# Kernel tuning notes

Measured on AMD Instinct MI355X. Metric: run time of the kernel, lower is better.

Reference implementation:

```python
import jax, jax.numpy as jnp
import numpy as np

TEMPERATURE = 0.07
EPS = 1e-12  # F.normalize eps


def setup_inputs() -> dict:
    key = jax.random.key(0)
    k1, k2 = jax.random.split(key)
    B, D = 4096, 1024
    return {
        "features_1": jax.random.normal(k1, (B, D), dtype=jnp.float32),
        "features_2": jax.random.normal(k2, (B, D), dtype=jnp.float32),
    }


def _l2_normalize(x):
    n = jnp.sqrt(jnp.sum(x * x, axis=1, keepdims=True))
    return x / jnp.maximum(n, EPS)


def reference(features_1, features_2):
    B = features_1.shape[0]
    f1 = _l2_normalize(features_1)
    f2 = _l2_normalize(features_2)
    f = jnp.concatenate([f1, f2], axis=0)  # [2B, D]
    # cosine sim of already-normalized vectors == plain matmul
    sim = (f @ f.T) / TEMPERATURE  # [2B, 2B]
    # denominator: logsumexp over each row excluding the diagonal (self-sim)
    eye = jnp.eye(2 * B, dtype=bool)
    lse = jax.nn.logsumexp(jnp.where(eye, -jnp.inf, sim), axis=1)  # [2B]
    # positives: cross-view pairs (i+B, i) then (i, i+B)
    idx = jnp.arange(B)
    pos = jnp.concatenate([sim[idx + B, idx], sim[idx, idx + B]], axis=0)  # [2B]
    loss = -jnp.mean(pos - lse)
    return loss
```

## Files before the change

kernel.cpp:

```cpp
#include <hip/hip_runtime.h>
#include <hip/hip_bf16.h>
#include <math.h>

#define INV_T (1.0f / 0.07f)

typedef __bf16 bf16x8 __attribute__((ext_vector_type(8)));
typedef float f32x4 __attribute__((ext_vector_type(4)));

__device__ __forceinline__ void gld16(const void* g, void* l) {
    __builtin_amdgcn_global_load_lds(
        (const __attribute__((address_space(1))) unsigned int*)g,
        (__attribute__((address_space(3))) unsigned int*)l,
        16, 0, 0);
}

__global__ __launch_bounds__(256) void norm_kernel(
    const float4* __restrict__ f1, const float4* __restrict__ f2,
    ushort4* __restrict__ F, float* __restrict__ S, float* __restrict__ P,
    int B) {
    const int i = blockIdx.x;
    const int t = threadIdx.x;

    float4 x = f1[i * 256 + t];
    float4 y = f2[i * 256 + t];

    float s1 = x.x * x.x + x.y * x.y + x.z * x.z + x.w * x.w;
    float s2 = y.x * y.x + y.y * y.y + y.z * y.z + y.w * y.w;
    float dd = x.x * y.x + x.y * y.y + x.z * y.z + x.w * y.w;

    for (int o = 32; o > 0; o >>= 1) {
        s1 += __shfl_down(s1, o);
        s2 += __shfl_down(s2, o);
        dd += __shfl_down(dd, o);
    }
    __shared__ float red[4][3];
    const int wv = t >> 6, ln = t & 63;
    if (ln == 0) { red[wv][0] = s1; red[wv][1] = s2; red[wv][2] = dd; }
    __syncthreads();
    s1 = red[0][0] + red[1][0] + red[2][0] + red[3][0];
    s2 = red[0][1] + red[1][1] + red[2][1] + red[3][1];
    dd = red[0][2] + red[1][2] + red[2][2] + red[3][2];

    const float rn1 = 1.0f / fmaxf(sqrtf(s1), 1e-12f);
    const float rn2 = 1.0f / fmaxf(sqrtf(s2), 1e-12f);

    union { ushort4 u; __hip_bfloat16 h[4]; } p;
    p.h[0] = __float2bfloat16(x.x * rn1);
    p.h[1] = __float2bfloat16(x.y * rn1);
    p.h[2] = __float2bfloat16(x.z * rn1);
    p.h[3] = __float2bfloat16(x.w * rn1);
    F[(size_t)i * 256 + t] = p.u;
    p.h[0] = __float2bfloat16(y.x * rn2);
    p.h[1] = __float2bfloat16(y.y * rn2);
    p.h[2] = __float2bfloat16(y.z * rn2);
    p.h[3] = __float2bfloat16(y.w * rn2);
    F[(size_t)(B + i) * 256 + t] = p.u;

    if (t == 0) {
        P[i] = dd * rn1 * rn2;
        S[i] = 0.0f;
        S[B + i] = 0.0f;
    }
}

__global__ __launch_bounds__(256, 2) void sim_kernel(
    const __hip_bfloat16* __restrict__ F, float* __restrict__ S,
    int N, int D) {
    __shared__ __align__(16) __hip_bfloat16 As[128][64];
    __shared__ __align__(16) __hip_bfloat16 Bs[256][64];

    const int k = blockIdx.x;
    int tj = (int)((sqrtf(4.0f * (float)k + 1.0f) - 1.0f) * 0.5f);
    while ((tj + 1) * (tj + 2) <= k) ++tj;
    while (tj * (tj + 1) > k) --tj;
    const int ti = k - tj * (tj + 1);
    const int bRow = ti * 128;
    const int bCol = tj * 256;

    const int tid  = threadIdx.x;
    const int wave = tid >> 6;
    const int lane = tid & 63;
    const int quad = lane >> 4;
    const int l16  = lane & 15;

    const int srow   = lane >> 3;
    const int ldsOff = (lane & 7) * 8;
    const int srcOff = ((lane & 7) ^ srow) * 8;

    const int waveRow = (wave >> 1) * 64;
    const int waveCol = (wave & 1) * 128;
    const int swz = l16 & 7;

    f32x4 acc[4][8];
#pragma unroll
    for (int mi = 0; mi < 4; ++mi)
#pragma unroll
        for (int ni = 0; ni < 8; ++ni)
            acc[mi][ni] = (f32x4){0.0f, 0.0f, 0.0f, 0.0f};

    for (int kb = 0; kb < D; kb += 64) {
#pragma unroll
        for (int p = 0; p < 4; ++p) {
            const int rowT = (p * 4 + wave) * 8 + srow;
            gld16(&F[(size_t)(bRow + rowT) * D + kb + srcOff], &As[rowT][ldsOff]);
        }
#pragma unroll
        for (int p = 0; p < 8; ++p) {
            const int rowT = (p * 4 + wave) * 8 + srow;
            gld16(&F[(size_t)(bCol + rowT) * D + kb + srcOff], &Bs[rowT][ldsOff]);
        }
        __syncthreads();

#pragma unroll
        for (int ks = 0; ks < 2; ++ks) {
            const int slot = ((ks * 4 + quad) ^ swz) * 8;
            bf16x8 bf[8];
#pragma unroll
            for (int ni = 0; ni < 8; ++ni)
                bf[ni] = *(const bf16x8*)&Bs[waveCol + ni * 16 + l16][slot];
#pragma unroll
            for (int mi = 0; mi < 4; ++mi) {
                const bf16x8 af = *(const bf16x8*)&As[waveRow + mi * 16 + l16][slot];
#pragma unroll
                for (int ni = 0; ni < 8; ++ni)
                    acc[mi][ni] = __builtin_amdgcn_mfma_f32_16x16x32_bf16(
                        af, bf[ni], acc[mi][ni], 0, 0, 0);
            }
        }
        __syncthreads();
    }

#pragma unroll
    for (int mi = 0; mi < 4; ++mi)
#pragma unroll
        for (int ni = 0; ni < 8; ++ni)
#pragma unroll
            for (int r = 0; r < 4; ++r) {
                const int gRow = bRow + waveRow + mi * 16 + quad * 4 + r;
                const int gCol = bCol + waveCol + ni * 16 + l16;
                acc[mi][ni][r] = (gRow < gCol)
                    ? __expf((acc[mi][ni][r] - 1.0f) * INV_T) : 0.0f;
            }

#pragma unroll
    for (int mi = 0; mi < 4; ++mi)
#pragma unroll
        for (int r = 0; r < 4; ++r) {
            const int gRow = bRow + waveRow + mi * 16 + quad * 4 + r;
            float v = 0.0f;
#pragma unroll
            for (int ni = 0; ni < 8; ++ni) v += acc[mi][ni][r];
            v += __shfl_xor(v, 1);
            v += __shfl_xor(v, 2);
            v += __shfl_xor(v, 4);
            v += __shfl_xor(v, 8);
            if (l16 == 0) atomicAdd(&S[gRow], v);
        }

#pragma unroll
    for (int ni = 0; ni < 8; ++ni) {
        float cv = 0.0f;
#pragma unroll
        for (int mi = 0; mi < 4; ++mi)
#pragma unroll
            for (int r = 0; r < 4; ++r) cv += acc[mi][ni][r];
        cv += __shfl_xor(cv, 16);
        cv += __shfl_xor(cv, 32);
        if (quad == 0) atomicAdd(&S[bCol + waveCol + ni * 16 + l16], cv);
    }
}

__global__ __launch_bounds__(256) void finalize_kernel(
    const float* __restrict__ S, const float* __restrict__ P,
    float* __restrict__ out, int N, int B) {
    float s = 0.0f;
    for (int i = threadIdx.x; i < N; i += 256) s += __logf(S[i]);
    float pp = 0.0f;
    for (int i = threadIdx.x; i < B; i += 256) pp += P[i];
    for (int o = 32; o > 0; o >>= 1) {
        s += __shfl_down(s, o);
        pp += __shfl_down(pp, o);
    }
    __shared__ float red[4][2];
    if ((threadIdx.x & 63) == 0) {
        red[threadIdx.x >> 6][0] = s;
        red[threadIdx.x >> 6][1] = pp;
    }
    __syncthreads();
    if (threadIdx.x == 0) {
        const float sl = red[0][0] + red[1][0] + red[2][0] + red[3][0];
        const float ps = red[0][1] + red[1][1] + red[2][1] + red[3][1];
        out[0] = INV_T + sl / (float)N - ps * (2.0f * INV_T / (float)N);
    }
}

extern "C" void kernel_launch(void* const* d_in, const int* in_sizes, int n_in,
                              void* d_out, int out_size, void* d_ws, size_t ws_size,
                              hipStream_t stream) {
    const int D = 1024;
    const int B = in_sizes[0] / D;
    const int N = 2 * B;
    const int M2 = N / 256;
    const int ntiles = M2 * M2 + M2;

    const float* f1 = (const float*)d_in[0];
    const float* f2 = (const float*)d_in[1];

    __hip_bfloat16* F = (__hip_bfloat16*)d_ws;
    float* S = (float*)((char*)d_ws + (size_t)N * D * sizeof(__hip_bfloat16));
    float* P = S + N;

    norm_kernel<<<dim3(B), dim3(256), 0, stream>>>(
        (const float4*)f1, (const float4*)f2, (ushort4*)F, S, P, B);
    sim_kernel<<<dim3(ntiles), dim3(256), 0, stream>>>(F, S, N, D);
    finalize_kernel<<<dim3(1), dim3(256), 0, stream>>>(S, P, (float*)d_out, N, B);
}
```

Before: 174.8 us.

## Rewrite sim GEMM as 256x256 tiles with double-buffered 8-wave pipeline

Replaces the 128x256 single-buffered sim kernel with 256x256 upper-triangular tiles computed by 512-thread blocks. Global-to-LDS loads are double-buffered and interleaved with MFMA phases, using explicit vmcnt waits, barriers and setprio. The goal is to hide memory latency behind MFMA work, raise arithmetic intensity, and cut the number of tiles and column atomics. In exchange it uses 128KB of LDS and heavy register pressure, which may limit occupancy, and the hand-scheduled barriers are fragile.

```diff
diff --git a/kernel.cpp b/kernel.cpp
--- a/kernel.cpp
+++ b/kernel.cpp
@@ -63,93 +63,161 @@
     }
 }
 
-__global__ __launch_bounds__(256, 2) void sim_kernel(
-    const __hip_bfloat16* __restrict__ F, float* __restrict__ S,
-    int N, int D) {
-    __shared__ __align__(16) __hip_bfloat16 As[128][64];
-    __shared__ __align__(16) __hip_bfloat16 Bs[256][64];
+
+#define BARRIER() asm volatile("s_barrier" ::: "memory")
+#define VMCNT6()  asm volatile("s_waitcnt vmcnt(6)" ::: "memory")
+#define VMCNT0()  asm volatile("s_waitcnt vmcnt(0)" ::: "memory")
+
+#define QUAD_MFMA(MH, NH)                                                     \
+    _Pragma("unroll") for (int mi = 0; mi < 4; ++mi)                          \
+    _Pragma("unroll") for (int ni = 0; ni < 2; ++ni)                          \
+    _Pragma("unroll") for (int ks = 0; ks < 2; ++ks)                          \
+        acc[(MH) * 4 + mi][(NH) * 2 + ni] =                                   \
+            __builtin_amdgcn_mfma_f32_16x16x32_bf16(                          \
+                af[mi][ks], bf[NH][ni][ks],                                   \
+                acc[(MH) * 4 + mi][(NH) * 2 + ni], 0, 0, 0);
+
+#define PH_COMPUTE(MH, NH)                                                    \
+    BARRIER();                                                                \
+    asm volatile("s_waitcnt lgkmcnt(0)" ::: "memory");                        \
+    __builtin_amdgcn_sched_barrier(0);                                        \
+    __builtin_amdgcn_s_setprio(1);                                            \
+    QUAD_MFMA(MH, NH);                                                        \
+    __builtin_amdgcn_s_setprio(0);                                            \
+    __builtin_amdgcn_sched_barrier(0);
+
+__global__ __launch_bounds__(512, 2) void sim_kernel(
+    const ushort* __restrict__ F, float* __restrict__ S, int N) {
+    (void)N;
+    __shared__ __align__(16) ushort lds[2][2][2][128 * 64];
 
     const int k = blockIdx.x;
-    int tj = (int)((sqrtf(4.0f * (float)k + 1.0f) - 1.0f) * 0.5f);
-    while ((tj + 1) * (tj + 2) <= k) ++tj;
-    while (tj * (tj + 1) > k) --tj;
-    const int ti = k - tj * (tj + 1);
-    const int bRow = ti * 128;
-    const int bCol = tj * 256;
-
-    const int tid  = threadIdx.x;
-    const int wave = tid >> 6;
-    const int lane = tid & 63;
-    const int quad = lane >> 4;
-    const int l16  = lane & 15;
-
-    const int srow   = lane >> 3;
-    const int ldsOff = (lane & 7) * 8;
-    const int srcOff = ((lane & 7) ^ srow) * 8;
-
-    const int waveRow = (wave >> 1) * 64;
-    const int waveCol = (wave & 1) * 128;
+    int tj = (int)((sqrtf(8.0f * (float)k + 1.0f) - 1.0f) * 0.5f);
+    while ((tj + 1) * (tj + 2) / 2 <= k) ++tj;
+    while (tj * (tj + 1) / 2 > k) --tj;
+    const int ti = k - tj * (tj + 1) / 2;
+    const int bRow = ti * 256, bCol = tj * 256;
+
+    const int tid = threadIdx.x;
+    const int wave = tid >> 6, lane = tid & 63;
+    const int wr = wave >> 2, wc = wave & 3;
+    const int quad = lane >> 4, l16 = lane & 15;
     const int swz = l16 & 7;
 
-    f32x4 acc[4][8];
-#pragma unroll
-    for (int mi = 0; mi < 4; ++mi)
-#pragma unroll
-        for (int ni = 0; ni < 8; ++ni)
-            acc[mi][ni] = (f32x4){0.0f, 0.0f, 0.0f, 0.0f};
-
-    for (int kb = 0; kb < D; kb += 64) {
-#pragma unroll
-        for (int p = 0; p < 4; ++p) {
-            const int rowT = (p * 4 + wave) * 8 + srow;
-            gld16(&F[(size_t)(bRow + rowT) * D + kb + srcOff], &As[rowT][ldsOff]);
-        }
-#pragma unroll
-        for (int p = 0; p < 8; ++p) {
-            const int rowT = (p * 4 + wave) * 8 + srow;
-            gld16(&F[(size_t)(bCol + rowT) * D + kb + srcOff], &Bs[rowT][ldsOff]);
-        }
-        __syncthreads();
-
-#pragma unroll
-        for (int ks = 0; ks < 2; ++ks) {
-            const int slot = ((ks * 4 + quad) ^ swz) * 8;
-            bf16x8 bf[8];
-#pragma unroll
-            for (int ni = 0; ni < 8; ++ni)
-                bf[ni] = *(const bf16x8*)&Bs[waveCol + ni * 16 + l16][slot];
-#pragma unroll
-            for (int mi = 0; mi < 4; ++mi) {
-                const bf16x8 af = *(const bf16x8*)&As[waveRow + mi * 16 + l16][slot];
-#pragma unroll
-                for (int ni = 0; ni < 8; ++ni)
-                    acc[mi][ni] = __builtin_amdgcn_mfma_f32_16x16x32_bf16(
-                        af, bf[ni], acc[mi][ni], 0, 0, 0);
+    const int r0 = tid >> 3;
+    const int scol = ((tid & 7) ^ (r0 & 7)) * 8;
+    const size_t gA = (size_t)(bRow + r0) * 1024 + scol;
+    const size_t gB = (size_t)(bCol + r0) * 1024 + scol;
+
+    auto stage = [&](int bsel, int ab, int h, int kb) {
+        const ushort* g = F + (ab ? gB : gA) + (size_t)h * (128 * 1024) + kb;
+        ushort* l = &lds[bsel][ab][h][tid * 8];
+        gld16(g, l);
+        gld16(g + 64 * 1024, l + 512 * 8);
+    };
+
+    bf16x8 af[4][2];
+    bf16x8 bf[2][2][2];
+    f32x4 acc[8][4];
+#pragma unroll
+    for (int a = 0; a < 8; ++a)
+#pragma unroll
+        for (int b = 0; b < 4; ++b) acc[a][b] = (f32x4){0.0f, 0.0f, 0.0f, 0.0f};
+
+    auto loadA = [&](int bsel, int mh) {
+#pragma unroll
+        for (int mi = 0; mi < 4; ++mi)
+#pragma unroll
+            for (int ks = 0; ks < 2; ++ks)
+                af[mi][ks] = *(const bf16x8*)&lds[bsel][0][wr]
+                    [(mh * 64 + mi * 16 + l16) * 64 + ((ks * 4 + quad) ^ swz) * 8];
+    };
+    auto loadB = [&](int bsel) {
+#pragma unroll
+        for (int nh = 0; nh < 2; ++nh)
+#pragma unroll
+            for (int ni = 0; ni < 2; ++ni)
+#pragma unroll
+                for (int ks = 0; ks < 2; ++ks)
+                    bf[nh][ni][ks] = *(const bf16x8*)&lds[bsel][1][wc >> 1]
+                        [((wc & 1) * 64 + nh * 32 + ni * 16 + l16) * 64 +
+                         ((ks * 4 + quad) ^ swz) * 8];
+    };
+
+    stage(0, 0, 0, 0); stage(0, 0, 1, 0); stage(0, 1, 0, 0); stage(0, 1, 1, 0);
+    stage(1, 1, 0, 64); stage(1, 1, 1, 64); stage(1, 0, 0, 64);
+    VMCNT6();
+    BARRIER();
+
+#pragma unroll 1
+    for (int it = 0; it < 7; ++it) {
+        const int kb0 = it * 128;
+        loadA(0, 0); loadB(0);
+        stage(1, 0, 1, kb0 + 64);
+        PH_COMPUTE(0, 0);
+        BARRIER();
+        stage(0, 1, 0, kb0 + 128);
+        PH_COMPUTE(0, 1);
+        BARRIER();
+        loadA(0, 1);
+        stage(0, 1, 1, kb0 + 128);
+        PH_COMPUTE(1, 0);
+        BARRIER();
+        stage(0, 0, 0, kb0 + 128);
+        PH_COMPUTE(1, 1);
+        VMCNT6();
+        BARRIER();
+        loadA(1, 0); loadB(1);
+        stage(0, 0, 1, kb0 + 128);
+        PH_COMPUTE(0, 0);
+        BARRIER();
+        stage(1, 1, 0, kb0 + 192);
+        PH_COMPUTE(0, 1);
+        BARRIER();
+        loadA(1, 1);
+        stage(1, 1, 1, kb0 + 192);
+        PH_COMPUTE(1, 0);
+        BARRIER();
+        stage(1, 0, 0, kb0 + 192);
+        PH_COMPUTE(1, 1);
+        VMCNT6();
+        BARRIER();
+    }
+
+    loadA(0, 0); loadB(0);
+    stage(1, 0, 1, 960);
+    QUAD_MFMA(0, 0);
+    QUAD_MFMA(0, 1);
+    loadA(0, 1);
+    QUAD_MFMA(1, 0);
+    QUAD_MFMA(1, 1);
+    VMCNT0();
+    BARRIER();
+    loadA(1, 0); loadB(1);
+    QUAD_MFMA(0, 0);
+    QUAD_MFMA(0, 1);
+    loadA(1, 1);
+    QUAD_MFMA(1, 0);
+    QUAD_MFMA(1, 1);
+
+#pragma unroll
+    for (int a = 0; a < 8; ++a)
+#pragma unroll
+        for (int b = 0; b < 4; ++b)
+#pragma unroll
+            for (int r = 0; r < 4; ++r) {
+                const int gRow = bRow + wr * 128 + (a >> 2) * 64 + (a & 3) * 16 + quad * 4 + r;
+                const int gCol = bCol + wc * 64 + (b >> 1) * 32 + (b & 1) * 16 + l16;
+                acc[a][b][r] = (gRow < gCol)
+                    ? __expf((acc[a][b][r] - 1.0f) * INV_T) : 0.0f;
             }
-        }
-        __syncthreads();
-    }
-
-#pragma unroll
-    for (int mi = 0; mi < 4; ++mi)
-#pragma unroll
-        for (int ni = 0; ni < 8; ++ni)
-#pragma unroll
-            for (int r = 0; r < 4; ++r) {
-                const int gRow = bRow + waveRow + mi * 16 + quad * 4 + r;
-                const int gCol = bCol + waveCol + ni * 16 + l16;
-                acc[mi][ni][r] = (gRow < gCol)
-                    ? __expf((acc[mi][ni][r] - 1.0f) * INV_T) : 0.0f;
-            }
-
-#pragma unroll
-    for (int mi = 0; mi < 4; ++mi)
+
+#pragma unroll
+    for (int a = 0; a < 8; ++a)
 #pragma unroll
         for (int r = 0; r < 4; ++r) {
-            const int gRow = bRow + waveRow + mi * 16 + quad * 4 + r;
-            float v = 0.0f;
-#pragma unroll
-            for (int ni = 0; ni < 8; ++ni) v += acc[mi][ni][r];
+            const int gRow = bRow + wr * 128 + (a >> 2) * 64 + (a & 3) * 16 + quad * 4 + r;
+            float v = acc[a][0][r] + acc[a][1][r] + acc[a][2][r] + acc[a][3][r];
             v += __shfl_xor(v, 1);
             v += __shfl_xor(v, 2);
             v += __shfl_xor(v, 4);
@@ -158,15 +226,18 @@
         }
 
 #pragma unroll
-    for (int ni = 0; ni < 8; ++ni) {
+    for (int b = 0; b < 4; ++b) {
         float cv = 0.0f;
 #pragma unroll
-        for (int mi = 0; mi < 4; ++mi)
-#pragma unroll
-            for (int r = 0; r < 4; ++r) cv += acc[mi][ni][r];
+        for (int a = 0; a < 8; ++a)
+#pragma unroll
+            for (int r = 0; r < 4; ++r) cv += acc[a][b][r];
         cv += __shfl_xor(cv, 16);
         cv += __shfl_xor(cv, 32);
-        if (quad == 0) atomicAdd(&S[bCol + waveCol + ni * 16 + l16], cv);
+        if (quad == 0) {
+            const int gCol = bCol + wc * 64 + (b >> 1) * 32 + (b & 1) * 16 + l16;
+            atomicAdd(&S[gCol], cv);
+        }
     }
 }
 
@@ -200,8 +271,8 @@
     const int D = 1024;
     const int B = in_sizes[0] / D;
     const int N = 2 * B;
-    const int M2 = N / 256;
-    const int ntiles = M2 * M2 + M2;
+    const int M = N / 256;
+    const int ntiles = M * (M + 1) / 2;
 
     const float* f1 = (const float*)d_in[0];
     const float* f2 = (const float*)d_in[1];
@@ -212,6 +283,6 @@
 
     norm_kernel<<<dim3(B), dim3(256), 0, stream>>>(
         (const float4*)f1, (const float4*)f2, (ushort4*)F, S, P, B);
-    sim_kernel<<<dim3(ntiles), dim3(256), 0, stream>>>(F, S, N, D);
+    sim_kernel<<<dim3(ntiles), dim3(512), 0, stream>>>((const ushort*)F, S, N);
     finalize_kernel<<<dim3(1), dim3(256), 0, stream>>>(S, P, (float*)d_out, N, B);
 }
```

Result: slower. 188.9 us (+8.1%).
